# Kernel tuning notes

Measured on AMD Instinct MI355X. Metric: run time of the kernel, lower is better.

## Reference

```python
import jax, jax.numpy as jnp
import numpy as np

NUM_CLASSES = 80
PRE_NMS_K = 400    # pre_nms_points / max_output_size_per_class
MAX_BOXES = 200    # max_total_size
NMS_THRESH = 0.6
SCORE_THRESH = 0.0  # iou_thresh in YoloLayer, used as score threshold/mask
SCALE_XY = (1.2, 1.1, 1.05)  # levels 3,4,5
STRIDES = (8.0, 16.0, 32.0)  # 2**level


def setup_inputs() -> dict:
    key = jax.random.key(0)
    k3, k4, k5 = jax.random.split(key, 3)
    B, C5 = 8, 3 * (NUM_CLASSES + 5)
    p3 = jax.random.normal(k3, (B, 64, 64, C5), dtype=jnp.float32)
    p4 = jax.random.normal(k4, (B, 32, 32, C5), dtype=jnp.float32)
    p5 = jax.random.normal(k5, (B, 16, 16, C5), dtype=jnp.float32)
    a3 = jnp.array([[12., 16.], [19., 36.], [40., 28.]], jnp.float32)
    a4 = jnp.array([[36., 75.], [76., 55.], [72., 146.]], jnp.float32)
    a5 = jnp.array([[142., 110.], [192., 243.], [459., 401.]], jnp.float32)
    return {"p3": p3, "p4": p4, "p5": p5, "a3": a3, "a4": a4, "a5": a5}


def _decode_level(p, anchors, stride, scale_xy):
    # p: [B,H,W,A*(C+5)] raw head output; 'original' box decode (sigmoid xy, exp wh)
    B, H, W, _ = p.shape
    A = anchors.shape[0]
    d = p.reshape(B, H, W, A, NUM_CLASSES + 5)
    txy, twh, tobj, tcls = d[..., :2], d[..., 2:4], d[..., 4:5], d[..., 5:]
    gx, gy = jnp.meshgrid(jnp.arange(W, dtype=p.dtype), jnp.arange(H, dtype=p.dtype))
    grid = jnp.stack([gx, gy], -1)[None, :, :, None, :]          # [1,H,W,1,2] (x,y)
    sxy = jnp.asarray(scale_xy, p.dtype)
    xy = (jax.nn.sigmoid(txy) * sxy - 0.5 * (sxy - 1.0) + grid) / jnp.array([W, H], p.dtype)
    wh = jnp.exp(twh) * anchors[None, None, None] / jnp.array([W * stride, H * stride], p.dtype)
    x1y1 = xy - 0.5 * wh
    x2y2 = xy + 0.5 * wh
    boxes = jnp.stack([x1y1[..., 1], x1y1[..., 0], x2y2[..., 1], x2y2[..., 0]], -1)  # yxyx
    obj = jax.nn.sigmoid(tobj)
    cls = jax.nn.sigmoid(tcls) * obj
    N = H * W * A
    return boxes.reshape(B, N, 4), cls.reshape(B, N, NUM_CLASSES), obj.reshape(B, N)


def _pairwise_iou(b):
    # b: [K,4] yxyx in [0,1]
    area = (b[:, 2] - b[:, 0]) * (b[:, 3] - b[:, 1])
    tl = jnp.maximum(b[:, None, :2], b[None, :, :2])
    br = jnp.minimum(b[:, None, 2:], b[None, :, 2:])
    wh = jnp.maximum(br - tl, 0.0)
    inter = wh[..., 0] * wh[..., 1]
    union = area[:, None] + area[None, :] - inter
    return inter / jnp.maximum(union, 1e-9)


def _greedy_nms_scores(boxes, scores):
    # boxes/scores already sorted by score descending; returns scores with suppressed -> 0
    K = scores.shape[0]
    overlap = _pairwise_iou(boxes) > NMS_THRESH
    idx = jnp.arange(K)

    def body(i, keep):
        sup = overlap[i] & (idx > i) & keep[i]
        return keep & ~sup

    keep = jax.lax.fori_loop(0, K, body, jnp.ones((K,), bool))
    return jnp.where(keep & (scores > SCORE_THRESH), scores, 0.0)


def _detections_per_image(boxes, cls_scores):
    # boxes [N,4], cls_scores [N,C] -> combined per-class NMS, top MAX_BOXES overall
    boxes = jnp.clip(boxes, 0.0, 1.0)  # combined NMS clips boxes by default

    def per_class(scores_c):
        vals, idx = jax.lax.top_k(scores_c, PRE_NMS_K)
        b = boxes[idx]
        return _greedy_nms_scores(b, vals), b

    kept_scores, kept_boxes = jax.vmap(per_class)(cls_scores.T)  # [C,K], [C,K,4]
    flat_s = kept_scores.reshape(-1)
    flat_b = kept_boxes.reshape(-1, 4)
    cls_ids = jnp.repeat(jnp.arange(NUM_CLASSES), PRE_NMS_K)
    top_s, top_i = jax.lax.top_k(flat_s, MAX_BOXES)
    top_b = flat_b[top_i]
    top_c = cls_ids[top_i].astype(jnp.float32)
    valid = top_s > 0.0
    top_b = jnp.where(valid[:, None], top_b, 0.0)
    top_c = jnp.where(valid, top_c, 0.0)
    num = jnp.sum(valid.astype(jnp.int32))
    return top_b, top_s, top_c, num


def _forward(p3, p4, p5, a3, a4, a5):
    boxes, cls_scores, obj_scores = [], [], []
    for (p, a), stride, sxy in zip(((p3, a3), (p4, a4), (p5, a5)), STRIDES, SCALE_XY):
        b, c, o = _decode_level(p, a, stride, sxy)
        boxes.append(b); cls_scores.append(c); obj_scores.append(o)
    boxes = jnp.concatenate(boxes, 1)            # [B,N,4]
    cls_scores = jnp.concatenate(cls_scores, 1)  # [B,N,C]
    obj_scores = jnp.concatenate(obj_scores, 1)  # [B,N]
    obj_mask = (obj_scores > SCORE_THRESH).astype(boxes.dtype)
    cls_mask = (cls_scores > SCORE_THRESH).astype(boxes.dtype)
    cls_scores = cls_scores * obj_mask[..., None] * cls_mask
    return jax.vmap(_detections_per_image)(boxes, cls_scores)


def reference(p3, p4, p5, a3, a4, a5):
    bbox, confidence, classes, num_detections = _forward(p3, p4, p5, a3, a4, a5)
    return bbox, confidence, classes, num_detections
```

## Files before the change

### kernel.cpp

```cpp
#include <hip/hip_runtime.h>
#include <math.h>

#define NCLS 80
#define PRE_K 400
#define MAX_BOXES 200
#define KEEP_CAP 200
#define N_TOT 16128
#define M_FIN (NCLS * KEEP_CAP)
#define NMS_T 0.6f
#define NTHR 512
#define NWAVE (NTHR / 64)
#define FTHR 512
#define CAP 512

typedef unsigned long long u64;
typedef unsigned int u32;
typedef unsigned short u16;

__device__ __forceinline__ float sigf(float x) { return 1.0f / (1.0f + expf(-x)); }

__device__ __forceinline__ float score_f32(int idx, int b, int c,
    const float* __restrict__ p3, const float* __restrict__ p4, const float* __restrict__ p5)
{
    const float* base; int W, n;
    if (idx < 12288)      { base = p3; W = 64; n = idx; }
    else if (idx < 15360) { base = p4; W = 32; n = idx - 12288; }
    else                  { base = p5; W = 16; n = idx - 15360; }
    int a = n % 3, hw = n / 3, w = hw % W, h = hw / W;
    const float* rec = base + (((b * W + h) * W + w) * 255 + a * 85);
    return sigf(rec[5 + c]) * sigf(rec[4]);
}

__device__ __forceinline__ void hist_agg(u32* hist, u32 d, bool valid, int lane)
{
    u64 act = __ballot(valid);
    while (act) {
        int ldr = __ffsll((unsigned long long)act) - 1;
        u32 dl = __shfl(d, ldr, 64);
        u64 m = __ballot(valid && d == dl);
        if (lane == ldr) atomicAdd(&hist[dl], (u32)__popcll(m));
        act &= ~m;
    }
}

__device__ __forceinline__ void digit_select(const u32* hist, int need,
                                             u32* sh_dg, u32* sh_S1, u32* sh_T, int tid)
{
    if (tid < 64) {
        const int lane = tid;
        u32 h0 = hist[4 * lane + 0], h1 = hist[4 * lane + 1];
        u32 h2 = hist[4 * lane + 2], h3 = hist[4 * lane + 3];
        u32 loc = h0 + h1 + h2 + h3;
        u32 s = loc;
#pragma unroll
        for (int off = 1; off < 64; off <<= 1) {
            u32 t = __shfl_down(s, off, 64);
            if (lane + off < 64) s += t;
        }
        u32 after = s - loc;
        u32 S3 = h3 + after, S2 = h2 + S3, S1v = h1 + S2, S0 = h0 + S1v;
        u32 Sarr[5] = { S0, S1v, S2, S3, after };
#pragma unroll
        for (int k = 0; k < 4; ++k) {
            if ((int)Sarr[k] >= need && need > (int)Sarr[k + 1]) {
                *sh_dg = (u32)(4 * lane + k);
                *sh_S1 = Sarr[k + 1];
                *sh_T  = Sarr[k] - Sarr[k + 1];
            }
        }
    }
    __syncthreads();
}

__device__ __forceinline__ void sort512(u64* cand, int tid)
{
    u64 v = cand[tid];
#pragma unroll
    for (int k2 = 2; k2 <= 64; k2 <<= 1) {
#pragma unroll
        for (int j = k2 >> 1; j > 0; j >>= 1) {
            u64 p = __shfl_xor(v, j, 64);
            bool takeMax = ((tid & k2) == 0) ^ ((tid & j) != 0);
            v = takeMax ? (v >= p ? v : p) : (v <= p ? v : p);
        }
    }
    for (int k2 = 128; k2 <= CAP; k2 <<= 1) {
        for (int j = k2 >> 1; j >= 64; j >>= 1) {
            __syncthreads();
            cand[tid] = v;
            __syncthreads();
            u64 p = cand[tid ^ j];
            bool takeMax = ((tid & k2) == 0) ^ ((tid & j) != 0);
            v = takeMax ? (v >= p ? v : p) : (v <= p ? v : p);
        }
#pragma unroll
        for (int j = 32; j > 0; j >>= 1) {
            u64 p = __shfl_xor(v, j, 64);
            bool takeMax = ((tid & k2) == 0) ^ ((tid & j) != 0);
            v = takeMax ? (v >= p ? v : p) : (v <= p ? v : p);
        }
    }
    __syncthreads();
    cand[tid] = v;
    __syncthreads();
}

__global__ __launch_bounds__(256) void decode_kernel(
    const float* __restrict__ p3, const float* __restrict__ p4, const float* __restrict__ p5,
    const float* __restrict__ a3, const float* __restrict__ a4, const float* __restrict__ a5,
    u16* __restrict__ scores16, float* __restrict__ boxes)
{
    const int blk = blockIdx.x;
    const int b = blk & 7;
    const int n = ((blk >> 3) << 8) + threadIdx.x;

    const float* base; const float* anc; int logw, nn; float sx;
    if (n < 12288)      { base = p3; anc = a3; logw = 6; nn = n;         sx = 1.2f;  }
    else if (n < 15360) { base = p4; anc = a4; logw = 5; nn = n - 12288; sx = 1.1f;  }
    else                { base = p5; anc = a5; logw = 4; nn = n - 15360; sx = 1.05f; }
    const int W = 1 << logw;
    const int a = nn % 3; const int hw = nn / 3;
    const int w = hw & (W - 1); const int h = hw >> logw;
    const float winv = 1.0f / (float)W;
    const float* rec = base + ((size_t)((b * W + h) * W + w) * 255 + a * 85);

    float tx = rec[0], ty = rec[1], tw = rec[2], th = rec[3], to = rec[4];
    float sobj = sigf(to);
    float cx = (sigf(tx) * sx - 0.5f * (sx - 1.0f) + (float)w) * winv;
    float cy = (sigf(ty) * sx - 0.5f * (sx - 1.0f) + (float)h) * winv;
    float bw = expf(tw) * anc[a * 2 + 0] * (1.0f / 512.0f);
    float bh = expf(th) * anc[a * 2 + 1] * (1.0f / 512.0f);
    float x1 = cx - 0.5f * bw, x2 = cx + 0.5f * bw;
    float y1 = cy - 0.5f * bh, y2 = cy + 0.5f * bh;
    y1 = fminf(fmaxf(y1, 0.f), 1.f); x1 = fminf(fmaxf(x1, 0.f), 1.f);
    y2 = fminf(fmaxf(y2, 0.f), 1.f); x2 = fminf(fmaxf(x2, 0.f), 1.f);
    float4 bb; bb.x = y1; bb.y = x1; bb.z = y2; bb.w = x2;
    ((float4*)boxes)[b * N_TOT + n] = bb;

    u16* sb = scores16 + (long)b * NCLS * N_TOT + n;
#pragma unroll 8
    for (int cc = 0; cc < NCLS; ++cc)
        sb[(long)cc * N_TOT] = (u16)(__float_as_uint(sigf(rec[5 + cc]) * sobj) >> 16);
}

__global__ __launch_bounds__(NTHR, 8) void topk_nms_fused(
    const u16* __restrict__ scores16, const float* __restrict__ boxes,
    const float* __restrict__ p3, const float* __restrict__ p4, const float* __restrict__ p5,
    float* __restrict__ ksc, float* __restrict__ kbox)
{
    __shared__ alignas(16) u64 cand[CAP];
    __shared__ u32 hist[260];
    __shared__ u32 sh_dg, sh_S1, sh_T;
    __shared__ int sh_gcnt;
    __shared__ alignas(16) float boxbuf[5 * 448];
    __shared__ alignas(16) u64 diagbuf[64];
    __shared__ u32 keepb[16];
    __shared__ u64 sh_keptM;
    __shared__ int wpre14[14];
    __shared__ int sh_ncnt;

    float* by1 = boxbuf;
    float* bx1 = boxbuf + 448;
    float* by2 = boxbuf + 896;
    float* bx2 = boxbuf + 1344;
    float* bar = boxbuf + 1792;

    const int tid = threadIdx.x;
    const int wv = tid >> 6;
    const int lane = tid & 63;
    const int b = blockIdx.x & 7;
    const int c = blockIdx.x >> 3;

    const u16* keys16g = scores16 + (long)(b * NCLS + c) * N_TOT;
    const uint4* k4g = (const uint4*)keys16g;
    const int N8 = N_TOT >> 3;

    if (tid < 260) hist[tid] = 0u;
    if (tid == 0) sh_gcnt = 0;
    __syncthreads();
#pragma unroll
    for (int it = 0; it < 4; ++it) {
        int i4 = tid + it * NTHR;
        bool v = i4 < N8;
        u32 e[8] = { 0,0,0,0,0,0,0,0 };
        if (v) {
            uint4 kk = k4g[i4];
            e[0] = kk.x & 0xffffu; e[1] = kk.x >> 16; e[2] = kk.y & 0xffffu; e[3] = kk.y >> 16;
            e[4] = kk.z & 0xffffu; e[5] = kk.z >> 16; e[6] = kk.w & 0xffffu; e[7] = kk.w >> 16;
        }
#pragma unroll
        for (int q = 0; q < 8; ++q) hist_agg(hist, e[q] >> 8, v, lane);
    }
    __syncthreads();

    int need = PRE_K;
    digit_select(hist, need, &sh_dg, &sh_S1, &sh_T, tid);
    u32 thr = sh_dg; need -= (int)sh_S1;
    int C = (PRE_K - need) + (int)sh_T;
    int lvl = 1;

    if (C > CAP) {
        if (tid < 256) hist[tid] = 0u;
        __syncthreads();
#pragma unroll
        for (int it = 0; it < 4; ++it) {
            int i4 = tid + it * NTHR;
            if (i4 < N8) {
                uint4 kk = k4g[i4];
                u32 e[8] = { kk.x & 0xffffu, kk.x >> 16, kk.y & 0xffffu, kk.y >> 16,
                             kk.z & 0xffffu, kk.z >> 16, kk.w & 0xffffu, kk.w >> 16 };
#pragma unroll
                for (int q = 0; q < 8; ++q)
                    if ((e[q] >> 8) == thr) atomicAdd(&hist[e[q] & 255u], 1u);
            }
        }
        __syncthreads();
        digit_select(hist, need, &sh_dg, &sh_S1, &sh_T, tid);
        thr = (thr << 8) | sh_dg; need -= (int)sh_S1;
        C = (PRE_K - need) + (int)sh_T;
        lvl = 2;
    }

    if (C > CAP) {
        u32 t16 = thr;
        if (tid < 256) hist[tid] = 0u;
        __syncthreads();
        for (int i = tid; i < N_TOT; i += NTHR) {
            if (keys16g[i] == (u16)t16) {
                u32 kb = __float_as_uint(score_f32(i, b, c, p3, p4, p5));
                atomicAdd(&hist[(kb >> 8) & 255u], 1u);
            }
        }
        __syncthreads();
        digit_select(hist, need, &sh_dg, &sh_S1, &sh_T, tid);
        thr = (thr << 8) | sh_dg; need -= (int)sh_S1;
        C = (PRE_K - need) + (int)sh_T;
        lvl = 3;
    }

    if (C > CAP) {
        u32 t16 = thr >> 8;
        if (tid < 256) hist[tid] = 0u;
        __syncthreads();
        for (int i = tid; i < N_TOT; i += NTHR) {
            if (keys16g[i] == (u16)t16) {
                u32 kb = __float_as_uint(score_f32(i, b, c, p3, p4, p5));
                if ((kb >> 8) == thr) atomicAdd(&hist[kb & 255u], 1u);
            }
        }
        __syncthreads();
        digit_select(hist, need, &sh_dg, &sh_S1, &sh_T, tid);
        thr = (thr << 8) | sh_dg; need -= (int)sh_S1;
        C = (PRE_K - need) + (int)sh_T;
        lvl = 4;
    }

    if (lvl <= 2) {
#pragma unroll
        for (int it = 0; it < 4; ++it) {
            int i4 = tid + it * NTHR;
            if (i4 < N8) {
                uint4 kk = k4g[i4];
                int i0 = i4 << 3;
                u32 e[8] = { kk.x & 0xffffu, kk.x >> 16, kk.y & 0xffffu, kk.y >> 16,
                             kk.z & 0xffffu, kk.z >> 16, kk.w & 0xffffu, kk.w >> 16 };
#pragma unroll
                for (int q = 0; q < 8; ++q) {
                    bool take = (lvl == 1) ? ((e[q] >> 8) >= thr) : (e[q] >= thr);
                    if (take) {
                        int p = atomicAdd(&sh_gcnt, 1);
                        int i = i0 + q;
                        u32 kb = __float_as_uint(score_f32(i, b, c, p3, p4, p5));
                        cand[p] = ((u64)kb << 32) | (u32)(0xFFFFFFFFu - (u32)i);
                    }
                }
            }
        }
        __syncthreads();
        for (int t = C + tid; t < CAP; t += NTHR) cand[t] = 0ull;
    } else if (C <= CAP) {
        u32 t16 = (lvl == 3) ? (thr >> 8) : (thr >> 16);
        for (int i = tid; i < N_TOT; i += NTHR) {
            u32 k = keys16g[i];
            bool take = false;
            u32 kb = 0;
            if (k > t16) { take = true; kb = __float_as_uint(score_f32(i, b, c, p3, p4, p5)); }
            else if (k == t16) {
                kb = __float_as_uint(score_f32(i, b, c, p3, p4, p5));
                take = (lvl == 3) ? ((kb >> 8) >= thr) : (kb >= thr);
            }
            if (take) {
                int p = atomicAdd(&sh_gcnt, 1);
                cand[p] = ((u64)kb << 32) | (u32)(0xFFFFFFFFu - (u32)i);
            }
        }
        __syncthreads();
        for (int t = C + tid; t < CAP; t += NTHR) cand[t] = 0ull;
    } else {
        u32 t16 = thr >> 16;
        for (int i = tid; i < N_TOT; i += NTHR) {
            u32 k = keys16g[i];
            if (k < t16) continue;
            u32 kb = __float_as_uint(score_f32(i, b, c, p3, p4, p5));
            if (kb > thr) {
                int p = atomicAdd(&sh_gcnt, 1);
                cand[p] = ((u64)kb << 32) | (u32)(0xFFFFFFFFu - (u32)i);
            }
        }
        __syncthreads();
        const int G = sh_gcnt;
        u32* scr = (u32*)boxbuf;
        int lo = tid * 32; if (lo > N_TOT) lo = N_TOT;
        int hi = lo + 32;  if (hi > N_TOT) hi = N_TOT;
        int lc = 0;
        for (int i = lo; i < hi; ++i)
            if (keys16g[i] == (u16)t16 &&
                __float_as_uint(score_f32(i, b, c, p3, p4, p5)) == thr) ++lc;
        u32* sc_cur = scr; u32* sc_oth = scr + NTHR;
        sc_cur[tid] = (u32)lc;
        __syncthreads();
        for (int off = 1; off < NTHR; off <<= 1) {
            sc_oth[tid] = sc_cur[tid] + ((tid >= off) ? sc_cur[tid - off] : 0u);
            __syncthreads();
            u32* tmp = sc_cur; sc_cur = sc_oth; sc_oth = tmp;
        }
        int r = (int)sc_cur[tid] - lc;
        for (int i = lo; i < hi; ++i) {
            if (keys16g[i] == (u16)t16 &&
                __float_as_uint(score_f32(i, b, c, p3, p4, p5)) == thr) {
                if (r < need) cand[G + r] = ((u64)thr << 32) | (u32)(0xFFFFFFFFu - (u32)i);
                ++r;
            }
        }
        __syncthreads();
        for (int t = PRE_K + tid; t < CAP; t += NTHR) cand[t] = 0ull;
    }
    __syncthreads();

    sort512(cand, tid);

    const float4* btab = (const float4*)boxes;
    for (int t = tid; t < 448; t += NTHR) {
        float y1 = 0.f, x1 = 0.f, y2 = 0.f, x2 = 0.f;
        if (t < PRE_K) {
            u64 key = cand[t];
            if ((key >> 32) != 0ull) {
                int idx = (int)(0xFFFFFFFFu - (u32)(key & 0xFFFFFFFFull));
                float4 bb = btab[b * N_TOT + idx];
                y1 = bb.x; x1 = bb.y; y2 = bb.z; x2 = bb.w;
            }
        }
        by1[t] = y1; bx1[t] = x1; by2[t] = y2; bx2[t] = x2;
        bar[t] = (y2 - y1) * (x2 - x1);
    }
    if (tid < 16) keepb[tid] = (tid < 12) ? 0xFFFFFFFFu : ((tid == 12) ? 0xFFFFu : 0u);
    __syncthreads();

    for (int ch = 0; ch < 7; ++ch) {
        const int rbase = ch << 6;
        const float ry1 = by1[rbase + lane], rx1v = bx1[rbase + lane];
        const float ry2 = by2[rbase + lane], rx2v = bx2[rbase + lane];
        const float ra  = bar[rbase + lane];

#pragma unroll
        for (int q = 0; q < 8; ++q) {
            const int rl = wv * 8 + q;
            const int rr = rbase + rl;
            u64 m = 0ull;
            bool rowAlive = (rr < PRE_K) && ((keepb[rr >> 5] >> (rr & 31)) & 1u);
            if (rowAlive) {
                float qy1 = by1[rr], qx1 = bx1[rr], qy2 = by2[rr], qx2 = bx2[rr], qa = bar[rr];
                float ty = fmaxf(qy1, ry1), tx = fmaxf(qx1, rx1v);
                float byv = fminf(qy2, ry2), rxv = fminf(qx2, rx2v);
                float inter = fmaxf(byv - ty, 0.f) * fmaxf(rxv - tx, 0.f);
                float uni = qa + ra - inter;
                bool o = (lane > rl) && ((inter / fmaxf(uni, 1e-9f)) > NMS_T);
                m = __ballot(o);
            }
            if (lane == 0) diagbuf[rl] = m;
        }
        __syncthreads();

        if (tid < 64) {
            u64 dgrow = diagbuf[lane];
            u64 kept = ((u64)keepb[2 * ch + 1] << 32) | (u64)keepb[2 * ch];
#pragma unroll 16
            for (int i = 0; i < 64; ++i) {
                u64 dgi = __shfl(dgrow, i);
                u64 msk = 0ull - ((kept >> i) & 1ull);
                kept &= ~(dgi & msk);
            }
            if (lane == 0) {
                sh_keptM = kept;
                keepb[2 * ch]     = (u32)(kept & 0xFFFFFFFFull);
                keepb[2 * ch + 1] = (u32)(kept >> 32);
            }
        }
        __syncthreads();

        {
            const u64 keptM = sh_keptM;
            if (keptM != 0ull) {
                for (int jj = rbase + 64 + wv; jj < PRE_K; jj += NWAVE) {
                    if ((keepb[jj >> 5] >> (jj & 31)) & 1u) {
                        float cy1 = by1[jj], cx1 = bx1[jj], cy2 = by2[jj], cx2 = bx2[jj], ca = bar[jj];
                        float ty = fmaxf(ry1, cy1), tx = fmaxf(rx1v, cx1);
                        float byv = fminf(ry2, cy2), rxv = fminf(rx2v, cx2);
                        float inter = fmaxf(byv - ty, 0.f) * fmaxf(rxv - tx, 0.f);
                        float uni = ra + ca - inter;
                        bool o = (inter / fmaxf(uni, 1e-9f)) > NMS_T;
                        u64 m = __ballot(o);
                        if ((m & keptM) != 0ull && lane == 0)
                            atomicAnd(&keepb[jj >> 5], ~(1u << (jj & 31)));
                    }
                }
            }
        }
        __syncthreads();
    }

    if (tid == 0) {
        int acc = 0;
        for (int w = 0; w < 14; ++w) { wpre14[w] = acc; acc += __popc(keepb[w]); }
        sh_ncnt = acc < KEEP_CAP ? acc : KEEP_CAP;
    }
    __syncthreads();

    const int blk_out = b * NCLS + c;
    float* osc = ksc + (long)blk_out * KEEP_CAP;
    float* obx = kbox + (long)blk_out * KEEP_CAP * 4;
    for (int t = tid; t < PRE_K; t += NTHR) {
        u32 kw = keepb[t >> 5];
        if ((kw >> (t & 31)) & 1u) {
            int pos = wpre14[t >> 5] + __popc(kw & ((1u << (t & 31)) - 1u));
            if (pos < KEEP_CAP) {
                osc[pos] = __uint_as_float((u32)(cand[t] >> 32));
                obx[pos * 4 + 0] = by1[t]; obx[pos * 4 + 1] = bx1[t];
                obx[pos * 4 + 2] = by2[t]; obx[pos * 4 + 3] = bx2[t];
            }
        }
    }
    for (int t = sh_ncnt + tid; t < KEEP_CAP; t += NTHR) {
        osc[t] = 0.0f;
        obx[t * 4 + 0] = 0.f; obx[t * 4 + 1] = 0.f;
        obx[t * 4 + 2] = 0.f; obx[t * 4 + 3] = 0.f;
    }
}

__device__ __forceinline__ void radix_topk_sort_f32(
    const u32* __restrict__ keys, int n, int K,
    u64* cand, u32* hist, u32* scr,
    u32* sh_dg, u32* sh_S1, u32* sh_T, int* sh_gcnt, int tid)
{
    int need = K;
    digit_select(hist, need, sh_dg, sh_S1, sh_T, tid);
    u32 thr = *sh_dg; need -= (int)*sh_S1;
    int C = (K - need) + (int)*sh_T;
    int eshift = 24;

    const uint4* k4 = (const uint4*)keys;
    const int n4 = n >> 2;
    const int nIter = (n4 + FTHR - 1) / FTHR;

    for (int shift = 16; shift >= 0 && C > CAP; shift -= 8) {
        if (tid < 256) hist[tid] = 0u;
        __syncthreads();
        for (int it = 0; it < nIter; ++it) {
            int i4 = tid + it * FTHR;
            if (i4 < n4) {
                uint4 kk = k4[i4];
                if ((kk.x >> (shift + 8)) == thr) atomicAdd(&hist[(kk.x >> shift) & 255u], 1u);
                if ((kk.y >> (shift + 8)) == thr) atomicAdd(&hist[(kk.y >> shift) & 255u], 1u);
                if ((kk.z >> (shift + 8)) == thr) atomicAdd(&hist[(kk.z >> shift) & 255u], 1u);
                if ((kk.w >> (shift + 8)) == thr) atomicAdd(&hist[(kk.w >> shift) & 255u], 1u);
            }
        }
        __syncthreads();
        digit_select(hist, need, sh_dg, sh_S1, sh_T, tid);
        thr = (thr << 8) | *sh_dg; need -= (int)*sh_S1;
        C = (K - need) + (int)*sh_T;
        eshift = shift;
    }

    if (C <= CAP) {
        for (int it = 0; it < nIter; ++it) {
            int i4 = tid + it * FTHR;
            if (i4 < n4) {
                uint4 kk = k4[i4];
                int i0 = i4 << 2;
                if ((kk.x >> eshift) >= thr) { int p = atomicAdd(sh_gcnt, 1); cand[p] = ((u64)kk.x << 32) | (u32)(0xFFFFFFFFu - (u32)(i0 + 0)); }
                if ((kk.y >> eshift) >= thr) { int p = atomicAdd(sh_gcnt, 1); cand[p] = ((u64)kk.y << 32) | (u32)(0xFFFFFFFFu - (u32)(i0 + 1)); }
                if ((kk.z >> eshift) >= thr) { int p = atomicAdd(sh_gcnt, 1); cand[p] = ((u64)kk.z << 32) | (u32)(0xFFFFFFFFu - (u32)(i0 + 2)); }
                if ((kk.w >> eshift) >= thr) { int p = atomicAdd(sh_gcnt, 1); cand[p] = ((u64)kk.w << 32) | (u32)(0xFFFFFFFFu - (u32)(i0 + 3)); }
            }
        }
        __syncthreads();
        for (int t = C + tid; t < CAP; t += FTHR) cand[t] = 0ull;
    } else {
        for (int i = tid; i < n; i += FTHR) {
            u32 k = keys[i];
            if (k > thr) {
                int p = atomicAdd(sh_gcnt, 1);
                cand[p] = ((u64)k << 32) | (u32)(0xFFFFFFFFu - (u32)i);
            }
        }
        __syncthreads();
        const int G = *sh_gcnt;
        int lo = tid * 32; if (lo > n) lo = n;
        int hi = lo + 32;  if (hi > n) hi = n;
        int lc = 0;
        for (int i = lo; i < hi; ++i) if (keys[i] == thr) ++lc;
        u32* sc_cur = scr; u32* sc_oth = scr + 512;
        sc_cur[tid] = (u32)lc;
        __syncthreads();
        for (int off = 1; off < FTHR; off <<= 1) {
            sc_oth[tid] = sc_cur[tid] + ((tid >= off) ? sc_cur[tid - off] : 0u);
            __syncthreads();
            u32* tmp = sc_cur; sc_cur = sc_oth; sc_oth = tmp;
        }
        int r = (int)sc_cur[tid] - lc;
        for (int i = lo; i < hi; ++i) {
            if (keys[i] == thr) {
                if (r < need) cand[G + r] = ((u64)thr << 32) | (u32)(0xFFFFFFFFu - (u32)i);
                ++r;
            }
        }
        __syncthreads();
        for (int t = K + tid; t < CAP; t += FTHR) cand[t] = 0ull;
    }
    __syncthreads();
    sort512(cand, tid);
}

__global__ __launch_bounds__(FTHR) void final_topk_kernel(
    const float* __restrict__ ksc, const float* __restrict__ kbox,
    float* __restrict__ out)
{
    __shared__ alignas(16) u64 cand[CAP];
    __shared__ u32 hist[260];
    __shared__ u32 scr[1024];
    __shared__ u32 sh_dg, sh_S1, sh_T;
    __shared__ int sh_gcnt;

    const int tid = threadIdx.x;
    const int lane = tid & 63;
    const int b = blockIdx.x;
    const u32* keys = (const u32*)(ksc + (long)b * M_FIN);

    if (tid < 260) hist[tid] = 0u;
    if (tid == 0) sh_gcnt = 0;
    __syncthreads();
    const uint4* k4 = (const uint4*)keys;
#pragma unroll
    for (int it = 0; it < 8; ++it) {
        int i4 = tid + it * FTHR;
        bool v = i4 < (M_FIN >> 2);
        u32 d0 = 0, d1 = 0, d2 = 0, d3 = 0;
        if (v) {
            uint4 kk = k4[i4];
            d0 = kk.x >> 24; d1 = kk.y >> 24; d2 = kk.z >> 24; d3 = kk.w >> 24;
        }
        hist_agg(hist, d0, v, lane);
        hist_agg(hist, d1, v, lane);
        hist_agg(hist, d2, v, lane);
        hist_agg(hist, d3, v, lane);
    }
    __syncthreads();

    radix_topk_sort_f32(keys, M_FIN, MAX_BOXES, cand, hist, scr,
                        &sh_dg, &sh_S1, &sh_T, &sh_gcnt, tid);

    float* obb = out;
    float* ocf = out + 8 * MAX_BOXES * 4;
    float* ocl = ocf + 8 * MAX_BOXES;
    float* onm = ocl + 8 * MAX_BOXES;

    float s = 0.f;
    if (tid < MAX_BOXES) {
        u64 key = cand[tid];
        s = __uint_as_float((u32)(key >> 32));
        float y1 = 0.f, x1 = 0.f, y2 = 0.f, x2 = 0.f, cid = 0.f;
        if (s > 0.0f) {
            int i = (int)(0xFFFFFFFFu - (u32)(key & 0xFFFFFFFFull));
            int cc = i / KEEP_CAP, j = i % KEEP_CAP;
            const float* bb = kbox + (((long)b * NCLS + cc) * KEEP_CAP + j) * 4;
            y1 = bb[0]; x1 = bb[1]; y2 = bb[2]; x2 = bb[3];
            cid = (float)cc;
        }
        long o = (long)b * MAX_BOXES + tid;
        obb[o * 4 + 0] = y1; obb[o * 4 + 1] = x1; obb[o * 4 + 2] = y2; obb[o * 4 + 3] = x2;
        ocf[o] = s; ocl[o] = cid;
    }
    int cnt = __syncthreads_count(tid < MAX_BOXES && s > 0.0f);
    if (tid == 0) onm[b] = (float)cnt;
}

extern "C" void kernel_launch(void* const* d_in, const int* in_sizes, int n_in,
                              void* d_out, int out_size, void* d_ws, size_t ws_size,
                              hipStream_t stream) {
    const float* p3 = (const float*)d_in[0];
    const float* p4 = (const float*)d_in[1];
    const float* p5 = (const float*)d_in[2];
    const float* a3 = (const float*)d_in[3];
    const float* a4 = (const float*)d_in[4];
    const float* a5 = (const float*)d_in[5];
    float* out = (float*)d_out;

    const size_t s16_bytes  = (size_t)8 * NCLS * N_TOT * 2;
    const size_t box_bytes  = (size_t)8 * N_TOT * 16;
    const size_t ksc_bytes  = (size_t)8 * NCLS * KEEP_CAP * 4;

    u16*   scores16 = (u16*)d_ws;
    float* boxes    = (float*)((char*)d_ws + s16_bytes);
    float* ksc      = (float*)((char*)d_ws + s16_bytes + box_bytes);
    float* kbox     = (float*)((char*)d_ws + s16_bytes + box_bytes + ksc_bytes);

    decode_kernel<<<504, 256, 0, stream>>>(p3, p4, p5, a3, a4, a5, scores16, boxes);
    topk_nms_fused<<<8 * NCLS, NTHR, 0, stream>>>(scores16, boxes, p3, p4, p5, ksc, kbox);
    final_topk_kernel<<<8, FTHR, 0, stream>>>(ksc, kbox, out);
}
```

Baseline: 185.7 us.

## Split top-k and NMS into separate kernels; use ballot-based 64-bin histograms

```diff
diff --git a/kernel.cpp b/kernel.cpp
--- a/kernel.cpp
+++ b/kernel.cpp
@@ -31,18 +31,6 @@
     return sigf(rec[5 + c]) * sigf(rec[4]);
 }
 
-__device__ __forceinline__ void hist_agg(u32* hist, u32 d, bool valid, int lane)
-{
-    u64 act = __ballot(valid);
-    while (act) {
-        int ldr = __ffsll((unsigned long long)act) - 1;
-        u32 dl = __shfl(d, ldr, 64);
-        u64 m = __ballot(valid && d == dl);
-        if (lane == ldr) atomicAdd(&hist[dl], (u32)__popcll(m));
-        act &= ~m;
-    }
-}
-
 __device__ __forceinline__ void digit_select(const u32* hist, int need,
                                              u32* sh_dg, u32* sh_S1, u32* sh_T, int tid)
 {
@@ -67,6 +55,28 @@
                 *sh_S1 = Sarr[k + 1];
                 *sh_T  = Sarr[k] - Sarr[k + 1];
             }
+        }
+    }
+    __syncthreads();
+}
+
+__device__ __forceinline__ void digit_select64(const u32* histw, int nwaves, int need,
+                                               u32* sh_dg, u32* sh_S1, u32* sh_T, int tid)
+{
+    if (tid < 64) {
+        const int lane = tid;
+        u32 tot = 0;
+        for (int w = 0; w < nwaves; ++w) tot += histw[w * 64 + lane];
+        u32 s = tot;
+#pragma unroll
+        for (int off = 1; off < 64; off <<= 1) {
+            u32 t = __shfl_down(s, off, 64);
+            if (lane + off < 64) s += t;
+        }
+        u32 Sd1 = __shfl_down(s, 1, 64);
+        if (lane == 63) Sd1 = 0;
+        if ((int)s >= need && need > (int)Sd1) {
+            *sh_dg = (u32)lane; *sh_S1 = Sd1; *sh_T = tot;
         }
     }
     __syncthreads();
@@ -143,27 +153,17 @@
         sb[(long)cc * N_TOT] = (u16)(__float_as_uint(sigf(rec[5 + cc]) * sobj) >> 16);
 }
 
-__global__ __launch_bounds__(NTHR, 8) void topk_nms_fused(
-    const u16* __restrict__ scores16, const float* __restrict__ boxes,
+__global__ __launch_bounds__(NTHR, 8) void topk_select(
+    const u16* __restrict__ scores16,
     const float* __restrict__ p3, const float* __restrict__ p4, const float* __restrict__ p5,
-    float* __restrict__ ksc, float* __restrict__ kbox)
+    u64* __restrict__ gcand)
 {
     __shared__ alignas(16) u64 cand[CAP];
     __shared__ u32 hist[260];
+    __shared__ u32 histw[NWAVE * 64];
+    __shared__ u32 scr[1024];
     __shared__ u32 sh_dg, sh_S1, sh_T;
     __shared__ int sh_gcnt;
-    __shared__ alignas(16) float boxbuf[5 * 448];
-    __shared__ alignas(16) u64 diagbuf[64];
-    __shared__ u32 keepb[16];
-    __shared__ u64 sh_keptM;
-    __shared__ int wpre14[14];
-    __shared__ int sh_ncnt;
-
-    float* by1 = boxbuf;
-    float* bx1 = boxbuf + 448;
-    float* by2 = boxbuf + 896;
-    float* bx2 = boxbuf + 1344;
-    float* bar = boxbuf + 1792;
 
     const int tid = threadIdx.x;
     const int wv = tid >> 6;
@@ -175,26 +175,40 @@
     const uint4* k4g = (const uint4*)keys16g;
     const int N8 = N_TOT >> 3;
 
-    if (tid < 260) hist[tid] = 0u;
     if (tid == 0) sh_gcnt = 0;
-    __syncthreads();
-#pragma unroll
-    for (int it = 0; it < 4; ++it) {
-        int i4 = tid + it * NTHR;
-        bool v = i4 < N8;
-        u32 e[8] = { 0,0,0,0,0,0,0,0 };
-        if (v) {
-            uint4 kk = k4g[i4];
-            e[0] = kk.x & 0xffffu; e[1] = kk.x >> 16; e[2] = kk.y & 0xffffu; e[3] = kk.y >> 16;
-            e[4] = kk.z & 0xffffu; e[5] = kk.z >> 16; e[6] = kk.w & 0xffffu; e[7] = kk.w >> 16;
-        }
-#pragma unroll
-        for (int q = 0; q < 8; ++q) hist_agg(hist, e[q] >> 8, v, lane);
+
+    {
+        u64 inv[6];
+#pragma unroll
+        for (int k = 0; k < 6; ++k) inv[k] = ((lane >> k) & 1) ? 0ull : ~0ull;
+        u32 cnt = 0;
+#pragma unroll
+        for (int it = 0; it < 4; ++it) {
+            int i4 = tid + it * NTHR;
+            bool v = i4 < N8;
+            uint4 kk; kk.x = 0u; kk.y = 0u; kk.z = 0u; kk.w = 0u;
+            if (v) kk = k4g[i4];
+            u64 mv = __ballot(v);
+            u32 e[8] = { kk.x & 0xffffu, kk.x >> 16, kk.y & 0xffffu, kk.y >> 16,
+                         kk.z & 0xffffu, kk.z >> 16, kk.w & 0xffffu, kk.w >> 16 };
+#pragma unroll
+            for (int q = 0; q < 8; ++q) {
+                u32 d = e[q] >> 8;
+                u64 macc = mv;
+#pragma unroll
+                for (int k = 0; k < 6; ++k) {
+                    u64 bk = __ballot(((d >> k) & 1) != 0);
+                    macc &= (bk ^ inv[k]);
+                }
+                cnt += (u32)__popcll(macc);
+            }
+        }
+        histw[wv * 64 + lane] = cnt;
     }
     __syncthreads();
 
     int need = PRE_K;
-    digit_select(hist, need, &sh_dg, &sh_S1, &sh_T, tid);
+    digit_select64(histw, NWAVE, need, &sh_dg, &sh_S1, &sh_T, tid);
     u32 thr = sh_dg; need -= (int)sh_S1;
     int C = (PRE_K - need) + (int)sh_T;
     int lvl = 1;
@@ -309,7 +323,6 @@
         }
         __syncthreads();
         const int G = sh_gcnt;
-        u32* scr = (u32*)boxbuf;
         int lo = tid * 32; if (lo > N_TOT) lo = N_TOT;
         int hi = lo + 32;  if (hi > N_TOT) hi = N_TOT;
         int lc = 0;
@@ -339,19 +352,44 @@
 
     sort512(cand, tid);
 
+    gcand[(long)blockIdx.x * CAP + tid] = cand[tid];
+}
+
+__global__ __launch_bounds__(NTHR, 8) void nms_compact(
+    const u64* __restrict__ gcand, const float* __restrict__ boxes,
+    float* __restrict__ ksc, float* __restrict__ kbox)
+{
+    __shared__ alignas(16) float boxbuf[5 * 448];
+    __shared__ alignas(16) u64 diagbuf[64];
+    __shared__ u32 keepb[16];
+    __shared__ u64 sh_keptM;
+    __shared__ int wpre14[14];
+    __shared__ int sh_ncnt;
+
+    float* by1 = boxbuf;
+    float* bx1 = boxbuf + 448;
+    float* by2 = boxbuf + 896;
+    float* bx2 = boxbuf + 1344;
+    float* bar = boxbuf + 1792;
+
+    const int tid = threadIdx.x;
+    const int wv = tid >> 6;
+    const int lane = tid & 63;
+    const int b = blockIdx.x & 7;
+    const int c = blockIdx.x >> 3;
+
+    const u64 ck = gcand[(long)blockIdx.x * CAP + tid];
+
     const float4* btab = (const float4*)boxes;
-    for (int t = tid; t < 448; t += NTHR) {
+    if (tid < 448) {
         float y1 = 0.f, x1 = 0.f, y2 = 0.f, x2 = 0.f;
-        if (t < PRE_K) {
-            u64 key = cand[t];
-            if ((key >> 32) != 0ull) {
-                int idx = (int)(0xFFFFFFFFu - (u32)(key & 0xFFFFFFFFull));
-                float4 bb = btab[b * N_TOT + idx];
-                y1 = bb.x; x1 = bb.y; y2 = bb.z; x2 = bb.w;
-            }
-        }
-        by1[t] = y1; bx1[t] = x1; by2[t] = y2; bx2[t] = x2;
-        bar[t] = (y2 - y1) * (x2 - x1);
+        if (tid < PRE_K && (ck >> 32) != 0ull) {
+            int idx = (int)(0xFFFFFFFFu - (u32)(ck & 0xFFFFFFFFull));
+            float4 bb = btab[b * N_TOT + idx];
+            y1 = bb.x; x1 = bb.y; y2 = bb.z; x2 = bb.w;
+        }
+        by1[tid] = y1; bx1[tid] = x1; by2[tid] = y2; bx2[tid] = x2;
+        bar[tid] = (y2 - y1) * (x2 - x1);
     }
     if (tid < 16) keepb[tid] = (tid < 12) ? 0xFFFFFFFFu : ((tid == 12) ? 0xFFFFu : 0u);
     __syncthreads();
@@ -429,14 +467,14 @@
     const int blk_out = b * NCLS + c;
     float* osc = ksc + (long)blk_out * KEEP_CAP;
     float* obx = kbox + (long)blk_out * KEEP_CAP * 4;
-    for (int t = tid; t < PRE_K; t += NTHR) {
-        u32 kw = keepb[t >> 5];
-        if ((kw >> (t & 31)) & 1u) {
-            int pos = wpre14[t >> 5] + __popc(kw & ((1u << (t & 31)) - 1u));
+    if (tid < PRE_K) {
+        u32 kw = keepb[tid >> 5];
+        if ((kw >> (tid & 31)) & 1u) {
+            int pos = wpre14[tid >> 5] + __popc(kw & ((1u << (tid & 31)) - 1u));
             if (pos < KEEP_CAP) {
-                osc[pos] = __uint_as_float((u32)(cand[t] >> 32));
-                obx[pos * 4 + 0] = by1[t]; obx[pos * 4 + 1] = bx1[t];
-                obx[pos * 4 + 2] = by2[t]; obx[pos * 4 + 3] = bx2[t];
+                osc[pos] = __uint_as_float((u32)(ck >> 32));
+                obx[pos * 4 + 0] = by1[tid]; obx[pos * 4 + 1] = bx1[tid];
+                obx[pos * 4 + 2] = by2[tid]; obx[pos * 4 + 3] = bx2[tid];
             }
         }
     }
@@ -449,13 +487,10 @@
 
 __device__ __forceinline__ void radix_topk_sort_f32(
     const u32* __restrict__ keys, int n, int K,
+    u32 thr, int need, int C,
     u64* cand, u32* hist, u32* scr,
     u32* sh_dg, u32* sh_S1, u32* sh_T, int* sh_gcnt, int tid)
 {
-    int need = K;
-    digit_select(hist, need, sh_dg, sh_S1, sh_T, tid);
-    u32 thr = *sh_dg; need -= (int)*sh_S1;
-    int C = (K - need) + (int)*sh_T;
     int eshift = 24;
 
     const uint4* k4 = (const uint4*)keys;
@@ -543,31 +578,48 @@
     __shared__ int sh_gcnt;
 
     const int tid = threadIdx.x;
+    const int wv = tid >> 6;
     const int lane = tid & 63;
     const int b = blockIdx.x;
     const u32* keys = (const u32*)(ksc + (long)b * M_FIN);
 
-    if (tid < 260) hist[tid] = 0u;
     if (tid == 0) sh_gcnt = 0;
-    __syncthreads();
     const uint4* k4 = (const uint4*)keys;
-#pragma unroll
-    for (int it = 0; it < 8; ++it) {
-        int i4 = tid + it * FTHR;
-        bool v = i4 < (M_FIN >> 2);
-        u32 d0 = 0, d1 = 0, d2 = 0, d3 = 0;
-        if (v) {
-            uint4 kk = k4[i4];
-            d0 = kk.x >> 24; d1 = kk.y >> 24; d2 = kk.z >> 24; d3 = kk.w >> 24;
-        }
-        hist_agg(hist, d0, v, lane);
-        hist_agg(hist, d1, v, lane);
-        hist_agg(hist, d2, v, lane);
-        hist_agg(hist, d3, v, lane);
-    }
-    __syncthreads();
-
-    radix_topk_sort_f32(keys, M_FIN, MAX_BOXES, cand, hist, scr,
+
+    {
+        u64 inv[6];
+#pragma unroll
+        for (int k = 0; k < 6; ++k) inv[k] = ((lane >> k) & 1) ? 0ull : ~0ull;
+        u32 cnt = 0;
+#pragma unroll
+        for (int it = 0; it < 8; ++it) {
+            int i4 = tid + it * FTHR;
+            bool v = i4 < (M_FIN >> 2);
+            uint4 kk; kk.x = 0u; kk.y = 0u; kk.z = 0u; kk.w = 0u;
+            if (v) kk = k4[i4];
+            u64 mv = __ballot(v);
+            u32 ds[4] = { kk.x >> 24, kk.y >> 24, kk.z >> 24, kk.w >> 24 };
+#pragma unroll
+            for (int q = 0; q < 4; ++q) {
+                u64 macc = mv;
+#pragma unroll
+                for (int k = 0; k < 6; ++k) {
+                    u64 bk = __ballot(((ds[q] >> k) & 1) != 0);
+                    macc &= (bk ^ inv[k]);
+                }
+                cnt += (u32)__popcll(macc);
+            }
+        }
+        scr[wv * 64 + lane] = cnt;
+    }
+    __syncthreads();
+
+    int need = MAX_BOXES;
+    digit_select64(scr, FTHR / 64, need, &sh_dg, &sh_S1, &sh_T, tid);
+    u32 thr = sh_dg; need -= (int)sh_S1;
+    int C = (MAX_BOXES - need) + (int)sh_T;
+
+    radix_topk_sort_f32(keys, M_FIN, MAX_BOXES, thr, need, C, cand, hist, scr,
                         &sh_dg, &sh_S1, &sh_T, &sh_gcnt, tid);
 
     float* obb = out;
@@ -609,13 +661,16 @@
     const size_t s16_bytes  = (size_t)8 * NCLS * N_TOT * 2;
     const size_t box_bytes  = (size_t)8 * N_TOT * 16;
     const size_t ksc_bytes  = (size_t)8 * NCLS * KEEP_CAP * 4;
+    const size_t kbox_bytes = (size_t)8 * NCLS * KEEP_CAP * 16;
 
     u16*   scores16 = (u16*)d_ws;
     float* boxes    = (float*)((char*)d_ws + s16_bytes);
     float* ksc      = (float*)((char*)d_ws + s16_bytes + box_bytes);
     float* kbox     = (float*)((char*)d_ws + s16_bytes + box_bytes + ksc_bytes);
+    u64*   gcand    = (u64*)((char*)d_ws + s16_bytes + box_bytes + ksc_bytes + kbox_bytes);
 
     decode_kernel<<<504, 256, 0, stream>>>(p3, p4, p5, a3, a4, a5, scores16, boxes);
-    topk_nms_fused<<<8 * NCLS, NTHR, 0, stream>>>(scores16, boxes, p3, p4, p5, ksc, kbox);
+    topk_select<<<8 * NCLS, NTHR, 0, stream>>>(scores16, p3, p4, p5, gcand);
+    nms_compact<<<8 * NCLS, NTHR, 0, stream>>>(gcand, boxes, ksc, kbox);
     final_topk_kernel<<<8, FTHR, 0, stream>>>(ksc, kbox, out);
 }
```

After: 195.1 us. 5.0% more time.
